# Kernel optimization log

Hardware: AMD Instinct MI355X
Metric: run time of the kernel (lower is better)

## Reference

```python
import jax, jax.numpy as jnp
import numpy as np

B, T, S, D_ENC, U, V_SZ = 16, 64, 128, 512, 256, 32000


def setup_inputs() -> dict:
    key = jax.random.key(0)
    ks = jax.random.split(key, 16)
    sc = lambda *sh: 1.0 / np.sqrt(sh[0])
    return {
        "dec_input": jax.random.randint(ks[0], (B, T), 0, V_SZ, dtype=jnp.int64),
        "enc_outputs": jax.random.normal(ks[1], (B, S, D_ENC), jnp.float32),
        "h0": jax.random.normal(ks[2], (B, U), jnp.float32),
        "c0": jax.random.normal(ks[3], (B, U), jnp.float32),
        "emb": jax.random.normal(ks[4], (V_SZ, U), jnp.float32) * 0.02,
        "W1": jax.random.normal(ks[5], (U, U), jnp.float32) * sc(U),
        "b1": jnp.zeros((U,), jnp.float32),
        "W2": jax.random.normal(ks[6], (D_ENC, U), jnp.float32) * sc(D_ENC),
        "b2": jnp.zeros((U,), jnp.float32),
        "Va": jax.random.normal(ks[7], (U, 1), jnp.float32) * sc(U),
        "bV": jnp.zeros((1,), jnp.float32),
        "Wx": jax.random.normal(ks[8], (D_ENC + U, 4 * U), jnp.float32) * sc(D_ENC + U),
        "Wh": jax.random.normal(ks[9], (U, 4 * U), jnp.float32) * sc(U),
        "b_lstm": jnp.zeros((4 * U,), jnp.float32),
        "Wd": jax.random.normal(ks[10], (U, V_SZ), jnp.float32) * sc(U),
        "bd": jnp.zeros((V_SZ,), jnp.float32),
    }


def reference(dec_input, enc_outputs, h0, c0, emb, W1, b1, W2, b2, Va, bV,
              Wx, Wh, b_lstm, Wd, bd):
    # Precompute W2(encoder_outputs): same math each step in the original.
    keys = enc_outputs @ W2 + b2                      # [B,S,U]

    def step(carry, tok):
        h, c = carry
        # Bahdanau attention, query = previous decoder hidden state
        q = h @ W1 + b1                               # [B,U]
        score = jnp.tanh(q[:, None, :] + keys) @ Va + bV   # [B,S,1]
        attn = jax.nn.softmax(score, axis=1)
        ctx = jnp.sum(attn * enc_outputs, axis=1)     # [B,D_ENC]
        # concat context with embedded token (teacher forcing)
        x = jnp.concatenate([ctx, emb[tok]], axis=-1)  # [B,D_ENC+U]
        # Keras LSTM cell: gate order i, f, g(c), o
        z = x @ Wx + h @ Wh + b_lstm                  # [B,4U]
        i, f, g, o = jnp.split(z, 4, axis=-1)
        c_new = jax.nn.sigmoid(f) * c + jax.nn.sigmoid(i) * jnp.tanh(g)
        h_new = jax.nn.sigmoid(o) * jnp.tanh(c_new)
        probs = jax.nn.softmax(h_new @ Wd + bd, axis=-1)   # [B,V]
        return (h_new, c_new), probs

    tokens = dec_input.T                              # [T,B]
    _, outs = jax.lax.scan(step, (h0, c0), tokens)    # [T,B,V]
    return jnp.transpose(outs, (1, 0, 2))             # [B,T,V]
```

## Files before the change

kernel.cpp:

```cpp
#include <hip/hip_runtime.h>


#define NB 16
#define NT 64
#define NS 128
#define DE 512
#define NU 256
#define NV 32000

static const size_t OFF_KEYS  = 0;
static const size_t OFF_HX    = 262144;
static const size_t OFF_PX    = 270336;
static const size_t OFF_RS    = 274432;
static const size_t OFF_CNT   = 275456;
static const size_t OFF_HB    = 275584;
static const size_t OFF_W1P   = 406656;
static const size_t OFF_ENCWX = 439424;
static const size_t OFF_ZEMB  = 2536576;
static const size_t OFF_WDT   = 3585152;

typedef __attribute__((ext_vector_type(8))) short bf16x8;
typedef __attribute__((ext_vector_type(4))) float f32x4;
typedef __attribute__((ext_vector_type(2))) _Float16 f16x2;

__device__ __forceinline__ float bf2f(unsigned int us) { return __uint_as_float(us << 16); }
__device__ __forceinline__ unsigned short f2bf(float f) {
    unsigned int u = __float_as_uint(f);
    return (unsigned short)((u + 0x7fffu + ((u >> 16) & 1u)) >> 16);
}
__device__ __forceinline__ float rcp_fast(float x) { return __builtin_amdgcn_rcpf(x); }
__device__ __forceinline__ float sigm(float x) { return rcp_fast(1.0f + __expf(-x)); }
__device__ __forceinline__ float tanh1(float x) {
    float e = __expf(2.0f * x);
    return 1.0f - 2.0f * rcp_fast(e + 1.0f);
}
__device__ __forceinline__ void cstore(float* p, float v) {
    __hip_atomic_store(p, v, __ATOMIC_RELAXED, __HIP_MEMORY_SCOPE_AGENT);
}
__device__ __forceinline__ float cload(const float* p) {
    return __hip_atomic_load(p, __ATOMIC_RELAXED, __HIP_MEMORY_SCOPE_AGENT);
}
__device__ __forceinline__ unsigned long long cload_ull(const unsigned long long* p) {
    return __hip_atomic_load(p, __ATOMIC_RELAXED, __HIP_MEMORY_SCOPE_AGENT);
}
__device__ __forceinline__ int cload_i(const int* p) {
    return __hip_atomic_load(p, __ATOMIC_RELAXED, __HIP_MEMORY_SCOPE_AGENT);
}

#if __has_builtin(__builtin_amdgcn_fdot2)
__device__ __forceinline__ float dot2(f16x2 w, f16x2 h, float a) {
    return __builtin_amdgcn_fdot2(w, h, a, false);
}
#else
__device__ __forceinline__ float dot2(f16x2 w, f16x2 h, float a) {
    return fmaf((float)w.x, (float)h.x, fmaf((float)w.y, (float)h.y, a));
}
#endif

__device__ __forceinline__ float poll_tagged(const float* p, unsigned tag) {
    float raw = cload(p);
    while ((__float_as_uint(raw) >> 31) != tag) {
        __builtin_amdgcn_s_sleep(1);
        raw = cload(p);
    }
    return __builtin_fabsf(raw);
}

__launch_bounds__(256)
__global__ void prologue_kernel(const int* __restrict__ dec, const float* __restrict__ enc,
                                const float* __restrict__ emb, const float* __restrict__ W1,
                                const float* __restrict__ W2, const float* __restrict__ b2,
                                const float* __restrict__ Wx, const float* __restrict__ b_lstm,
                                float* __restrict__ rs, int* __restrict__ cnt,
                                float* __restrict__ hx, float* __restrict__ px,
                                unsigned int* __restrict__ W1h, unsigned short* __restrict__ keysT,
                                float* __restrict__ encWx, float* __restrict__ zemb) {
    int blk = blockIdx.x, tid = threadIdx.x;
    if (blk < 4) {
        int i = blk * 256 + tid;
        rs[i] = 0.f;
        if (i < 128) cnt[i] = 0;
    } else if (blk < 52) {
        int idx = (blk - 4) * 256 + tid;
        if (idx < 4096) hx[idx] = 2.0f;
        else if (idx < 8192) hx[idx] = -2.0f;
        else px[idx - 8192] = -1.0f;
    } else if (blk < 180) {
        int id = (blk - 52) * 256 + tid;
        int dp = id >> 8, u = id & 255;
        unsigned short lo = __builtin_bit_cast(unsigned short, (_Float16)W1[(size_t)(2 * dp) * NU + u]);
        unsigned short hi = __builtin_bit_cast(unsigned short, (_Float16)W1[(size_t)(2 * dp + 1) * NU + u]);
        W1h[id] = (unsigned int)lo | ((unsigned int)hi << 16);
    } else if (blk < 308) {
        int bb = (blk - 180) >> 3, sg = (blk - 180) & 7;
        int u = tid;
        float acc[16];
        float bias = b2[u];
#pragma unroll
        for (int r = 0; r < 16; r++) acc[r] = bias;
        const float4* e4 = (const float4*)(enc + ((size_t)bb * NS + sg * 16) * DE);
        const float* wp = W2 + u;
        for (int k4 = 0; k4 < DE / 4; k4++) {
            float w0 = wp[(size_t)(k4 * 4 + 0) * NU];
            float w1 = wp[(size_t)(k4 * 4 + 1) * NU];
            float w2v = wp[(size_t)(k4 * 4 + 2) * NU];
            float w3v = wp[(size_t)(k4 * 4 + 3) * NU];
#pragma unroll
            for (int r = 0; r < 16; r++) {
                float4 e = e4[(size_t)r * (DE / 4) + k4];
                acc[r] = fmaf(e.x, w0, fmaf(e.y, w1, fmaf(e.z, w2v, fmaf(e.w, w3v, acc[r]))));
            }
        }
        unsigned int ow[8];
#pragma unroll
        for (int i = 0; i < 8; i++)
            ow[i] = (unsigned int)f2bf(acc[2 * i]) | ((unsigned int)f2bf(acc[2 * i + 1]) << 16);
        uint4* dst = (uint4*)(keysT + ((size_t)bb * NU + u) * NS + sg * 16);
        dst[0] = make_uint4(ow[0], ow[1], ow[2], ow[3]);
        dst[1] = make_uint4(ow[4], ow[5], ow[6], ow[7]);
    } else if (blk < 820) {
        int rg = (blk - 308) >> 2, jq = (blk - 308) & 3;
        int j = jq * 256 + tid;
        float acc[16];
#pragma unroll
        for (int r = 0; r < 16; r++) acc[r] = 0.f;
        const float4* e4 = (const float4*)(enc + (size_t)rg * 16 * DE);
        const float* wp = Wx + j;
        for (int k4 = 0; k4 < DE / 4; k4++) {
            float w0 = wp[(size_t)(k4 * 4 + 0) * 1024];
            float w1 = wp[(size_t)(k4 * 4 + 1) * 1024];
            float w2v = wp[(size_t)(k4 * 4 + 2) * 1024];
            float w3v = wp[(size_t)(k4 * 4 + 3) * 1024];
#pragma unroll
            for (int r = 0; r < 16; r++) {
                float4 e = e4[(size_t)r * (DE / 4) + k4];
                acc[r] = fmaf(e.x, w0, fmaf(e.y, w1, fmaf(e.z, w2v, fmaf(e.w, w3v, acc[r]))));
            }
        }
#pragma unroll
        for (int r = 0; r < 16; r++) encWx[(size_t)(rg * 16 + r) * 1024 + j] = acc[r];
    } else {
        int rg = (blk - 820) >> 2, jq = (blk - 820) & 3;
        int j = jq * 256 + tid;
        int tokr[16];
#pragma unroll
        for (int r = 0; r < 16; r++) {
            int row = rg * 16 + r;
            int tok = dec[(row >> 6) * NT + (row & 63)];
            tokr[r] = (tok < 0) ? 0 : (tok >= NV ? NV - 1 : tok);
        }
        float acc[16];
        float bias = b_lstm[j];
#pragma unroll
        for (int r = 0; r < 16; r++) acc[r] = bias;
        const float* wp = Wx + (size_t)512 * 1024 + j;
        for (int k4 = 0; k4 < NU / 4; k4++) {
            float w0 = wp[(size_t)(k4 * 4 + 0) * 1024];
            float w1 = wp[(size_t)(k4 * 4 + 1) * 1024];
            float w2v = wp[(size_t)(k4 * 4 + 2) * 1024];
            float w3v = wp[(size_t)(k4 * 4 + 3) * 1024];
#pragma unroll
            for (int r = 0; r < 16; r++) {
                float4 e = ((const float4*)(emb + (size_t)tokr[r] * NU))[k4];
                acc[r] = fmaf(e.x, w0, fmaf(e.y, w1, fmaf(e.z, w2v, fmaf(e.w, w3v, acc[r]))));
            }
        }
#pragma unroll
        for (int r = 0; r < 16; r++) zemb[(size_t)(rg * 16 + r) * 1024 + j] = acc[r];
    }
}

__launch_bounds__(256)
__global__ void wdtile_kernel(const float* __restrict__ Wd, unsigned short* __restrict__ wdT) {
    int id = blockIdx.x * 256 + threadIdx.x;
    int l = id & 63, c16 = (id >> 6) & 7, ks = (id >> 9) & 7, p = id >> 12;
    int v = p * 128 + c16 * 16 + (l & 15);
    int k0 = ks * 32 + (l >> 4) * 8;
    unsigned int wout[4];
#pragma unroll
    for (int jj = 0; jj < 4; jj++) {
        unsigned int lo = f2bf(Wd[(size_t)(k0 + 2 * jj) * NV + v]);
        unsigned int hi = f2bf(Wd[(size_t)(k0 + 2 * jj + 1) * NV + v]);
        wout[jj] = lo | (hi << 16);
    }
    *(uint4*)(wdT + (size_t)id * 8) = make_uint4(wout[0], wout[1], wout[2], wout[3]);
}

__launch_bounds__(512, 2)
__global__ void mega_kernel(const float* __restrict__ b1, const float* __restrict__ Va,
                            const float* __restrict__ bV, const float* __restrict__ Wh,
                            const float* __restrict__ h0, const float* __restrict__ c0,
                            const unsigned short* __restrict__ keysT,
                            const unsigned int* __restrict__ W1h,
                            const float* __restrict__ encWx, const float* __restrict__ zemb,
                            float* __restrict__ hx, float* __restrict__ px,
                            unsigned short* __restrict__ Hb,
                            const unsigned short* __restrict__ wdT,
                            const float* __restrict__ bd, float* __restrict__ rs,
                            int* __restrict__ cnt, float* __restrict__ out) {
    __shared__ float smem[21504];
    int tid = threadIdx.x;
    int blk = blockIdx.x;
    int xcd = blk & 7;
    int slot = blk >> 3;
    int* pdone = cnt;
    int* done0 = cnt + 32;

    if (xcd < 4) {
        int b = (slot >> 3) * 4 + xcd;
        int r = slot & 7;

        float* hl = smem;
        _Float16* hf = (_Float16*)(smem + 256);
        float* qred = smem + 384;
        float* qv = smem + 896;
        float* scp = smem + 1152;
        float* attnp = smem + 1664;
        float* zred = smem + 1792;

        int kg = tid >> 7, jl = tid & 127;
        int g = jl >> 5, i32 = jl & 31;
        int j = g * 256 + r * 32 + i32;

        float bV0 = bV[0];
        float c_reg = (tid < 32) ? c0[b * NU + r * 32 + tid] : 0.f;

        float wreg[96];
        {
            const float* ew = encWx + (size_t)b * 128 * 1024 + j;
            const float* wh = Wh + j;
#pragma unroll
            for (int kk = 0; kk < 96; kk++) {
                int k = kg * 96 + kk;
                wreg[kk] = (k < 128) ? ew[(size_t)k * 1024] : wh[(size_t)(k - 128) * 1024];
            }
        }

        for (int it = 0; it < NT; ++it) {
            unsigned tag = (unsigned)((it >> 1) & 1);
            float zpre4[4];
            if (tid < 32) {
#pragma unroll
                for (int gg = 0; gg < 4; gg++)
                    zpre4[gg] = zemb[((size_t)b * NT + it) * 1024 + gg * 256 + r * 32 + tid];
            }
            if (tid < NU) {
                float hv;
                if (it == 0) {
                    hv = h0[b * NU + tid];
                } else {
                    hv = poll_tagged(hx + (size_t)(it & 1) * 4096 + b * NU + tid, tag) - 2.0f;
                }
                hl[tid] = hv;
                hf[tid] = (_Float16)hv;
            }
            __syncthreads();

            {
                int u0 = tid & 255, dh = tid >> 8;
                const unsigned int* wp = W1h + dh * 64 * 256 + u0;
                const f16x2* hp = (const f16x2*)hf + dh * 64;
                float a = 0.f;
#pragma unroll 8
                for (int dp = 0; dp < 64; dp++) {
                    f16x2 wv = __builtin_bit_cast(f16x2, wp[(size_t)dp * 256]);
                    a = dot2(wv, hp[dp], a);
                }
                qred[dh * 256 + u0] = a;
            }
            __syncthreads();
            if (tid < NU) qv[tid] = qred[tid] + qred[256 + tid] + b1[tid];
            __syncthreads();

            {
                int sl = tid & 15, uc = tid >> 4;
                int s = r * 16 + sl;
                const unsigned short* kp = keysT + ((size_t)b * NU + uc * 8) * NS + s;
                float sc = 0.f;
#pragma unroll
                for (int i = 0; i < 8; i++)
                    sc = fmaf(tanh1(qv[uc * 8 + i] + bf2f(kp[(size_t)i * NS])), Va[uc * 8 + i], sc);
                scp[uc * 16 + sl] = sc;
            }
            __syncthreads();
            if (tid < 16) {
                float sum = bV0;
#pragma unroll
                for (int k = 0; k < 32; k++) sum += scp[k * 16 + tid];
                float p = __expf(sum);
                cstore(px + (size_t)(it & 1) * 2048 + b * NS + r * 16 + tid, tag ? -p : p);
            }
            float aH = 0.f;
            if (kg == 1) {
#pragma unroll
                for (int kk = 32; kk < 96; kk++) aH = fmaf(wreg[kk], hl[kk - 32], aH);
            } else if (kg >= 2) {
                int base = kg * 96 - 128;
#pragma unroll
                for (int kk = 0; kk < 96; kk++) aH = fmaf(wreg[kk], hl[base + kk], aH);
            }
            if (tid < 128) {
                attnp[tid] = poll_tagged(px + (size_t)(it & 1) * 2048 + b * NS + tid, tag);
            }
            __syncthreads();
            float tot;
            {
                int lane = tid & 63;
                float v = attnp[lane] + attnp[64 + lane];
#pragma unroll
                for (int off = 32; off >= 1; off >>= 1) v += __shfl_xor(v, off, 64);
                tot = v;
            }
            float aA = 0.f;
            if (kg == 0) {
#pragma unroll
                for (int kk = 0; kk < 96; kk++) aA = fmaf(wreg[kk], attnp[kk], aA);
            } else if (kg == 1) {
#pragma unroll
                for (int kk = 0; kk < 32; kk++) aA = fmaf(wreg[kk], attnp[96 + kk], aA);
            }
            zred[kg * 128 + jl] = aA * rcp_fast(tot) + aH;
            __syncthreads();

            if (tid < 32) {
                float z4[4];
#pragma unroll
                for (int gg = 0; gg < 4; gg++) {
                    int jj = gg * 32 + tid;
                    z4[gg] = zred[jj] + zred[128 + jj] + zred[256 + jj] + zred[384 + jj] + zpre4[gg];
                }
                float cn = sigm(z4[1]) * c_reg + sigm(z4[0]) * tanh1(z4[2]);
                c_reg = cn;
                float hn = sigm(z4[3]) * tanh1(cn);
                int u = r * 32 + tid;
                int rr = it * NB + b;
                int mp = rr >> 7, lr = rr & 127;
                int chunk = ((u >> 5) * 8 + (lr >> 4)) * 64 + ((u >> 3) & 3) * 16 + (lr & 15);
                __hip_atomic_store(&Hb[(size_t)mp * 32768 + chunk * 8 + (u & 7)], f2bf(hn),
                                   __ATOMIC_RELAXED, __HIP_MEMORY_SCOPE_AGENT);
                unsigned ntag = (unsigned)(((it + 1) >> 1) & 1);
                float enc2 = hn + 2.0f;
                cstore(hx + (size_t)((it + 1) & 1) * 4096 + b * NU + u, ntag ? -enc2 : enc2);
            }
            if ((it & 7) == 7 && tid < 64) {
                asm volatile("s_waitcnt vmcnt(0)" ::: "memory");
                if (tid == 0)
                    __hip_atomic_fetch_add(pdone + (it >> 3), 1, __ATOMIC_RELAXED,
                                           __HIP_MEMORY_SCOPE_AGENT);
            }
        }
    } else {
        int c = slot * 4 + (xcd - 4);
        float* ldsA = smem;
        float* sums = smem + 16384;
        const unsigned long long* HbU = (const unsigned long long*)Hb;
        unsigned long long* ldsU = (unsigned long long*)ldsA;

        int wave = tid >> 6, l = tid & 63;
        int wm = wave >> 2, wn = wave & 3;
        int nt = (c < 122) ? 2 : 1;

        for (int p = 0; p < 8; p++) {
            if (tid == 0)
                while (cload_i(pdone + p) < 128) __builtin_amdgcn_s_sleep(32);
            __syncthreads();
            for (int i = tid; i < 8192; i += 512)
                ldsU[i] = cload_ull(HbU + (size_t)p * 8192 + i);
            __syncthreads();

            f32x4 acc[2][4][2];
            float bdv[2][2];
            const bf16x8* A = (const bf16x8*)ldsA;
#pragma unroll
            for (int t = 0; t < 2; t++) {
                if (t >= nt) break;
                int np = c + 128 * t;
                const bf16x8* B = (const bf16x8*)wdT + (size_t)np * 4096;
#pragma unroll
                for (int mf = 0; mf < 4; mf++)
#pragma unroll
                    for (int nf = 0; nf < 2; nf++) acc[t][mf][nf] = (f32x4){0.f, 0.f, 0.f, 0.f};
#pragma unroll
                for (int ks = 0; ks < 8; ks++) {
                    bf16x8 av[4], bv[2];
#pragma unroll
                    for (int mf = 0; mf < 4; mf++) av[mf] = A[(ks * 8 + wm * 4 + mf) * 64 + l];
#pragma unroll
                    for (int nf = 0; nf < 2; nf++) bv[nf] = B[(ks * 8 + wn * 2 + nf) * 64 + l];
#pragma unroll
                    for (int mf = 0; mf < 4; mf++)
#pragma unroll
                        for (int nf = 0; nf < 2; nf++)
                            acc[t][mf][nf] = __builtin_amdgcn_mfma_f32_16x16x32_bf16(
                                av[mf], bv[nf], acc[t][mf][nf], 0, 0, 0);
                }
#pragma unroll
                for (int nf = 0; nf < 2; nf++)
                    bdv[t][nf] = bd[np * 128 + wn * 32 + nf * 16 + (l & 15)];
#pragma unroll
                for (int mf = 0; mf < 4; mf++) {
#pragma unroll
                    for (int reg = 0; reg < 4; reg++) {
                        float v = __expf(acc[t][mf][0][reg] + bdv[t][0]) +
                                  __expf(acc[t][mf][1][reg] + bdv[t][1]);
                        v += __shfl_xor(v, 1);
                        v += __shfl_xor(v, 2);
                        v += __shfl_xor(v, 4);
                        v += __shfl_xor(v, 8);
                        if ((l & 15) == 0) {
                            int row = wm * 64 + mf * 16 + (l >> 4) * 4 + reg;
                            if (t == 0) sums[row * 4 + wn] = v;
                            else sums[row * 4 + wn] += v;
                        }
                    }
                }
            }
            __syncthreads();
            if (tid < 128) {
                float s = sums[tid * 4] + sums[tid * 4 + 1] + sums[tid * 4 + 2] + sums[tid * 4 + 3];
                atomicAdd(&rs[p * 128 + tid], s);
            }
            asm volatile("s_waitcnt vmcnt(0)" ::: "memory");
            __syncthreads();
            if (tid == 0) {
                __hip_atomic_fetch_add(done0 + p, 1, __ATOMIC_RELAXED, __HIP_MEMORY_SCOPE_AGENT);
                while (cload_i(done0 + p) < 128) __builtin_amdgcn_s_sleep(8);
            }
            __syncthreads();

            float rinv[4][4];
#pragma unroll
            for (int mf = 0; mf < 4; mf++)
#pragma unroll
                for (int reg = 0; reg < 4; reg++)
                    rinv[mf][reg] =
                        1.0f / cload(&rs[p * 128 + wm * 64 + mf * 16 + (l >> 4) * 4 + reg]);
#pragma unroll
            for (int t = 0; t < 2; t++) {
                if (t >= nt) break;
                int np = c + 128 * t;
#pragma unroll
                for (int mf = 0; mf < 4; mf++) {
#pragma unroll
                    for (int nf = 0; nf < 2; nf++) {
                        int col = np * 128 + wn * 32 + nf * 16 + (l & 15);
#pragma unroll
                        for (int reg = 0; reg < 4; reg++) {
                            int rr = p * 128 + wm * 64 + mf * 16 + (l >> 4) * 4 + reg;
                            float pv = __expf(acc[t][mf][nf][reg] + bdv[t][nf]);
                            out[(size_t)((rr & 15) * NT + (rr >> 4)) * NV + col] =
                                pv * rinv[mf][reg];
                        }
                    }
                }
            }
        }
    }
}

extern "C" void kernel_launch(void* const* d_in, const int* in_sizes, int n_in,
                              void* d_out, int out_size, void* d_ws, size_t ws_size,
                              hipStream_t stream) {
    const int* dec = (const int*)d_in[0];
    const float* enc = (const float*)d_in[1];
    const float* h0 = (const float*)d_in[2];
    const float* c0 = (const float*)d_in[3];
    const float* emb = (const float*)d_in[4];
    const float* W1 = (const float*)d_in[5];
    const float* b1 = (const float*)d_in[6];
    const float* W2 = (const float*)d_in[7];
    const float* b2 = (const float*)d_in[8];
    const float* Va = (const float*)d_in[9];
    const float* bV = (const float*)d_in[10];
    const float* Wx = (const float*)d_in[11];
    const float* Wh = (const float*)d_in[12];
    const float* b_lstm = (const float*)d_in[13];
    const float* Wd = (const float*)d_in[14];
    const float* bd = (const float*)d_in[15];
    float* out = (float*)d_out;
    float* ws = (float*)d_ws;

    unsigned short* keysT = (unsigned short*)(ws + OFF_KEYS);
    float* hx = ws + OFF_HX;
    float* px = ws + OFF_PX;
    float* ws_rs = ws + OFF_RS;
    int* cnt = (int*)(ws + OFF_CNT);
    unsigned short* Hb = (unsigned short*)(ws + OFF_HB);
    unsigned int* W1h = (unsigned int*)(ws + OFF_W1P);
    float* encWx = ws + OFF_ENCWX;
    float* zemb = ws + OFF_ZEMB;
    unsigned short* wdT = (unsigned short*)(ws + OFF_WDT);

    prologue_kernel<<<1076, 256, 0, stream>>>(dec, enc, emb, W1, W2, b2, Wx, b_lstm,
                                              ws_rs, cnt, hx, px, W1h, keysT, encWx, zemb);
    wdtile_kernel<<<4000, 256, 0, stream>>>(Wd, wdT);

    void* args[] = {(void*)&b1, (void*)&Va, (void*)&bV, (void*)&Wh, (void*)&h0, (void*)&c0,
                    (void*)&keysT, (void*)&W1h, (void*)&encWx, (void*)&zemb, (void*)&hx,
                    (void*)&px, (void*)&Hb, (void*)&wdT, (void*)&bd, (void*)&ws_rs,
                    (void*)&cnt, (void*)&out};
    hipLaunchCooperativeKernel((const void*)mega_kernel, dim3(256), dim3(512), args, 0, stream);
}
```

Before: 476.5 us.

## Compute attention scores locally per block and fold Wd tiling into prologue

Each block of the persistent mega kernel previously computed a 16-position slice of attention scores and exchanged them through tagged global memory polling. Now every block computes all 128 scores for its batch row locally, which removes the cross-block publish and poll step at the cost of redundant tanh work. Separately, the Wd bf16 tiling kernel is merged into the prologue launch to save one kernel launch. The h-projection accumulation is moved after the score computation.

```diff
diff --git a/kernel.cpp b/kernel.cpp
--- a/kernel.cpp
+++ b/kernel.cpp
@@ -10,7 +10,6 @@
 
 static const size_t OFF_KEYS  = 0;
 static const size_t OFF_HX    = 262144;
-static const size_t OFF_PX    = 270336;
 static const size_t OFF_RS    = 274432;
 static const size_t OFF_CNT   = 275456;
 static const size_t OFF_HB    = 275584;
@@ -71,28 +70,28 @@
                                 const float* __restrict__ emb, const float* __restrict__ W1,
                                 const float* __restrict__ W2, const float* __restrict__ b2,
                                 const float* __restrict__ Wx, const float* __restrict__ b_lstm,
+                                const float* __restrict__ Wd,
                                 float* __restrict__ rs, int* __restrict__ cnt,
-                                float* __restrict__ hx, float* __restrict__ px,
+                                float* __restrict__ hx,
                                 unsigned int* __restrict__ W1h, unsigned short* __restrict__ keysT,
-                                float* __restrict__ encWx, float* __restrict__ zemb) {
+                                float* __restrict__ encWx, float* __restrict__ zemb,
+                                unsigned short* __restrict__ wdT) {
     int blk = blockIdx.x, tid = threadIdx.x;
     if (blk < 4) {
         int i = blk * 256 + tid;
         rs[i] = 0.f;
         if (i < 128) cnt[i] = 0;
-    } else if (blk < 52) {
+    } else if (blk < 36) {
         int idx = (blk - 4) * 256 + tid;
-        if (idx < 4096) hx[idx] = 2.0f;
-        else if (idx < 8192) hx[idx] = -2.0f;
-        else px[idx - 8192] = -1.0f;
-    } else if (blk < 180) {
-        int id = (blk - 52) * 256 + tid;
+        hx[idx] = (idx < 4096) ? 2.0f : -2.0f;
+    } else if (blk < 164) {
+        int id = (blk - 36) * 256 + tid;
         int dp = id >> 8, u = id & 255;
         unsigned short lo = __builtin_bit_cast(unsigned short, (_Float16)W1[(size_t)(2 * dp) * NU + u]);
         unsigned short hi = __builtin_bit_cast(unsigned short, (_Float16)W1[(size_t)(2 * dp + 1) * NU + u]);
         W1h[id] = (unsigned int)lo | ((unsigned int)hi << 16);
-    } else if (blk < 308) {
-        int bb = (blk - 180) >> 3, sg = (blk - 180) & 7;
+    } else if (blk < 292) {
+        int bb = (blk - 164) >> 3, sg = (blk - 164) & 7;
         int u = tid;
         float acc[16];
         float bias = b2[u];
@@ -118,8 +117,8 @@
         uint4* dst = (uint4*)(keysT + ((size_t)bb * NU + u) * NS + sg * 16);
         dst[0] = make_uint4(ow[0], ow[1], ow[2], ow[3]);
         dst[1] = make_uint4(ow[4], ow[5], ow[6], ow[7]);
-    } else if (blk < 820) {
-        int rg = (blk - 308) >> 2, jq = (blk - 308) & 3;
+    } else if (blk < 804) {
+        int rg = (blk - 292) >> 2, jq = (blk - 292) & 3;
         int j = jq * 256 + tid;
         float acc[16];
 #pragma unroll
@@ -139,8 +138,8 @@
         }
 #pragma unroll
         for (int r = 0; r < 16; r++) encWx[(size_t)(rg * 16 + r) * 1024 + j] = acc[r];
-    } else {
-        int rg = (blk - 820) >> 2, jq = (blk - 820) & 3;
+    } else if (blk < 1060) {
+        int rg = (blk - 804) >> 2, jq = (blk - 804) & 3;
         int j = jq * 256 + tid;
         int tokr[16];
 #pragma unroll
@@ -167,23 +166,20 @@
         }
 #pragma unroll
         for (int r = 0; r < 16; r++) zemb[(size_t)(rg * 16 + r) * 1024 + j] = acc[r];
+    } else {
+        int id = (blk - 1060) * 256 + tid;
+        int l = id & 63, c16 = (id >> 6) & 7, ks = (id >> 9) & 7, p = id >> 12;
+        int v = p * 128 + c16 * 16 + (l & 15);
+        int k0 = ks * 32 + (l >> 4) * 8;
+        unsigned int wout[4];
+#pragma unroll
+        for (int jj = 0; jj < 4; jj++) {
+            unsigned int lo = f2bf(Wd[(size_t)(k0 + 2 * jj) * NV + v]);
+            unsigned int hi = f2bf(Wd[(size_t)(k0 + 2 * jj + 1) * NV + v]);
+            wout[jj] = lo | (hi << 16);
+        }
+        *(uint4*)(wdT + (size_t)id * 8) = make_uint4(wout[0], wout[1], wout[2], wout[3]);
     }
-}
-
-__launch_bounds__(256)
-__global__ void wdtile_kernel(const float* __restrict__ Wd, unsigned short* __restrict__ wdT) {
-    int id = blockIdx.x * 256 + threadIdx.x;
-    int l = id & 63, c16 = (id >> 6) & 7, ks = (id >> 9) & 7, p = id >> 12;
-    int v = p * 128 + c16 * 16 + (l & 15);
-    int k0 = ks * 32 + (l >> 4) * 8;
-    unsigned int wout[4];
-#pragma unroll
-    for (int jj = 0; jj < 4; jj++) {
-        unsigned int lo = f2bf(Wd[(size_t)(k0 + 2 * jj) * NV + v]);
-        unsigned int hi = f2bf(Wd[(size_t)(k0 + 2 * jj + 1) * NV + v]);
-        wout[jj] = lo | (hi << 16);
-    }
-    *(uint4*)(wdT + (size_t)id * 8) = make_uint4(wout[0], wout[1], wout[2], wout[3]);
 }
 
 __launch_bounds__(512, 2)
@@ -193,8 +189,7 @@
                             const unsigned short* __restrict__ keysT,
                             const unsigned int* __restrict__ W1h,
                             const float* __restrict__ encWx, const float* __restrict__ zemb,
-                            float* __restrict__ hx, float* __restrict__ px,
-                            unsigned short* __restrict__ Hb,
+                            float* __restrict__ hx, unsigned short* __restrict__ Hb,
                             const unsigned short* __restrict__ wdT,
                             const float* __restrict__ bd, float* __restrict__ rs,
                             int* __restrict__ cnt, float* __restrict__ out) {
@@ -273,34 +268,19 @@
             __syncthreads();
 
             {
-                int sl = tid & 15, uc = tid >> 4;
-                int s = r * 16 + sl;
-                const unsigned short* kp = keysT + ((size_t)b * NU + uc * 8) * NS + s;
+                int s = tid & 127, uc = tid >> 7;
+                const unsigned short* kp = keysT + ((size_t)b * NU + uc * 64) * NS + s;
                 float sc = 0.f;
-#pragma unroll
-                for (int i = 0; i < 8; i++)
-                    sc = fmaf(tanh1(qv[uc * 8 + i] + bf2f(kp[(size_t)i * NS])), Va[uc * 8 + i], sc);
-                scp[uc * 16 + sl] = sc;
-            }
-            __syncthreads();
-            if (tid < 16) {
-                float sum = bV0;
-#pragma unroll
-                for (int k = 0; k < 32; k++) sum += scp[k * 16 + tid];
-                float p = __expf(sum);
-                cstore(px + (size_t)(it & 1) * 2048 + b * NS + r * 16 + tid, tag ? -p : p);
-            }
-            float aH = 0.f;
-            if (kg == 1) {
-#pragma unroll
-                for (int kk = 32; kk < 96; kk++) aH = fmaf(wreg[kk], hl[kk - 32], aH);
-            } else if (kg >= 2) {
-                int base = kg * 96 - 128;
-#pragma unroll
-                for (int kk = 0; kk < 96; kk++) aH = fmaf(wreg[kk], hl[base + kk], aH);
-            }
+#pragma unroll 4
+                for (int i = 0; i < 64; i++)
+                    sc = fmaf(tanh1(qv[uc * 64 + i] + bf2f(kp[(size_t)i * NS])),
+                              Va[uc * 64 + i], sc);
+                scp[uc * 128 + s] = sc;
+            }
+            __syncthreads();
             if (tid < 128) {
-                attnp[tid] = poll_tagged(px + (size_t)(it & 1) * 2048 + b * NS + tid, tag);
+                float sum = scp[tid] + scp[128 + tid] + scp[256 + tid] + scp[384 + tid] + bV0;
+                attnp[tid] = __expf(sum);
             }
             __syncthreads();
             float tot;
@@ -311,13 +291,19 @@
                 for (int off = 32; off >= 1; off >>= 1) v += __shfl_xor(v, off, 64);
                 tot = v;
             }
-            float aA = 0.f;
+            float aA = 0.f, aH = 0.f;
             if (kg == 0) {
 #pragma unroll
                 for (int kk = 0; kk < 96; kk++) aA = fmaf(wreg[kk], attnp[kk], aA);
             } else if (kg == 1) {
 #pragma unroll
                 for (int kk = 0; kk < 32; kk++) aA = fmaf(wreg[kk], attnp[96 + kk], aA);
+#pragma unroll
+                for (int kk = 32; kk < 96; kk++) aH = fmaf(wreg[kk], hl[kk - 32], aH);
+            } else {
+                int base = kg * 96 - 128;
+#pragma unroll
+                for (int kk = 0; kk < 96; kk++) aH = fmaf(wreg[kk], hl[base + kk], aH);
             }
             zred[kg * 128 + jl] = aA * rcp_fast(tot) + aH;
             __syncthreads();
@@ -482,7 +468,6 @@
 
     unsigned short* keysT = (unsigned short*)(ws + OFF_KEYS);
     float* hx = ws + OFF_HX;
-    float* px = ws + OFF_PX;
     float* ws_rs = ws + OFF_RS;
     int* cnt = (int*)(ws + OFF_CNT);
     unsigned short* Hb = (unsigned short*)(ws + OFF_HB);
@@ -491,13 +476,12 @@
     float* zemb = ws + OFF_ZEMB;
     unsigned short* wdT = (unsigned short*)(ws + OFF_WDT);
 
-    prologue_kernel<<<1076, 256, 0, stream>>>(dec, enc, emb, W1, W2, b2, Wx, b_lstm,
-                                              ws_rs, cnt, hx, px, W1h, keysT, encWx, zemb);
-    wdtile_kernel<<<4000, 256, 0, stream>>>(Wd, wdT);
+    prologue_kernel<<<5060, 256, 0, stream>>>(dec, enc, emb, W1, W2, b2, Wx, b_lstm, Wd,
+                                              ws_rs, cnt, hx, W1h, keysT, encWx, zemb, wdT);
 
     void* args[] = {(void*)&b1, (void*)&Va, (void*)&bV, (void*)&Wh, (void*)&h0, (void*)&c0,
                     (void*)&keysT, (void*)&W1h, (void*)&encWx, (void*)&zemb, (void*)&hx,
-                    (void*)&px, (void*)&Hb, (void*)&wdT, (void*)&bd, (void*)&ws_rs,
+                    (void*)&Hb, (void*)&wdT, (void*)&bd, (void*)&ws_rs,
                     (void*)&cnt, (void*)&out};
     hipLaunchCooperativeKernel((const void*)mega_kernel, dim3(256), dim3(512), args, 0, stream);
 }
```

Measured after the change: 601.0 us. 1.26x slower.
